# Kernel optimization log

Hardware: AMD Instinct MI355X
Metric: run time of the kernel (lower is better)

The kernel has to match this reference:

```python
import jax, jax.numpy as jnp
import numpy as np

N_SAMPLES = 16384
IN_FEATURES = 2048
N_COMPONENTS = 512
MAX_CROSS_TERMS = 512
# With n_components=512, max_cross_terms=512: interaction_depth=2 -> only pairwise
# cross terms, and n_pairwise = min(512*511//2, 512) = 512 (the first 512 pairs in
# lexicographic (i, j), i<j order -- exactly what the chunked torch loops produce).
_pi, _pj = np.triu_indices(N_COMPONENTS, k=1)  # lexicographic row-major order
PAIR_I = jnp.asarray(_pi[:MAX_CROSS_TERMS])
PAIR_J = jnp.asarray(_pj[:MAX_CROSS_TERMS])
SQRT_EPS = 1e-8


def setup_inputs() -> dict:
    key = jax.random.key(0)
    k1, k2 = jax.random.split(key)
    X = jax.random.normal(k1, (N_SAMPLES, IN_FEATURES), dtype=jnp.float32)
    projection = jax.random.normal(k2, (IN_FEATURES, N_COMPONENTS), dtype=jnp.float32) / np.sqrt(N_COMPONENTS)
    return {"X": X, "projection": projection}


def reference(X, projection):
    # Random projection: [N, in] @ [in, C] -> [N, C]
    Xp = X @ projection
    n = X.shape[0]
    bias = jnp.ones((n, 1), dtype=X.dtype)                 # 'bias' chunk
    p1 = Xp                                                # power_1
    p2 = Xp * Xp                                           # power_2
    p3 = p2 * Xp                                           # power_3
    pairs = Xp[:, PAIR_I] * Xp[:, PAIR_J]                  # pairwise cross terms
    sq = jnp.sqrt(jnp.abs(Xp) + SQRT_EPS)                  # sqrt features
    # Feature layout matches torch offsets: bias | p1 | p2 | p3 | cross | sqrt
    return jnp.concatenate([bias, p1, p2, p3, pairs, sq], axis=1)  # [N, 2561]
```

## Files before the change

kernel.cpp:

```cpp
#include <hip/hip_runtime.h>
#include <hip/hip_bf16.h>
#include <math.h>


typedef __attribute__((ext_vector_type(4))) float f32x4;
typedef __attribute__((ext_vector_type(8))) short bf16x8;

#define MM 16384
#define NN 512
#define KK 2048
#define OUTW 2561

#define BM 128
#define BN 128
#define BK 32
#define NT (KK / BK)

__device__ __forceinline__ short f2bf(float x) {
  union { __hip_bfloat16 b; short s; } u;
  u.b = __float2bfloat16(x);
  return u.s;
}

__device__ __forceinline__ bf16x8 cvt8(f32x4 a, f32x4 b) {
  bf16x8 r;
  r[0] = f2bf(a[0]); r[1] = f2bf(a[1]); r[2] = f2bf(a[2]); r[3] = f2bf(a[3]);
  r[4] = f2bf(b[0]); r[5] = f2bf(b[1]); r[6] = f2bf(b[2]); r[7] = f2bf(b[3]);
  return r;
}

__device__ __forceinline__ void gl_lds16(const void* g, void* l) {
  __builtin_amdgcn_global_load_lds((const __attribute__((address_space(1))) unsigned int*)g,
                                   (__attribute__((address_space(3))) unsigned int*)l, 16, 0, 0);
}

__global__ __launch_bounds__(256) void prep_b(const float* __restrict__ P, short* __restrict__ Bt) {
  __shared__ float ts[64][65];
  const int tid = threadIdx.x;
  const int k0 = (blockIdx.x >> 3) * 64;
  const int n0 = (blockIdx.x & 7) * 64;
#pragma unroll
  for (int j = 0; j < 16; ++j) {
    int idx = j * 256 + tid;
    int kr = idx >> 6, nc = idx & 63;
    ts[kr][nc] = P[(size_t)(k0 + kr) * NN + n0 + nc];
  }
  __syncthreads();
#pragma unroll
  for (int j = 0; j < 16; ++j) {
    int idx = j * 256 + tid;
    int nr = idx >> 6, kc = idx & 63;
    Bt[(size_t)(n0 + nr) * KK + k0 + kc] = f2bf(ts[kc][nr]);
  }
}

__global__ __launch_bounds__(256) void gemm4(const float* __restrict__ X,
                                             const short* __restrict__ Bt,
                                             float* __restrict__ out) {
  __shared__ short As[2][BM * BK];
  __shared__ short Bs[2][BN * BK];

  const int tid = threadIdx.x;
  const int wid = tid >> 6, lane = tid & 63;
  const int lrow = lane & 15, kh = lane >> 4;
  const int wr = wid >> 1, wc = wid & 1;

  const int bid = blockIdx.x;
  const int tile = (bid & 7) * 64 + (bid >> 3);
  const int m0 = (tile >> 2) * BM;
  const int n0 = (tile & 3) * BN;

  const int ar0 = tid >> 2, akq = tid & 3;
  const float* aG = X + (size_t)(m0 + ar0) * KK + akq * 8;
  int aoff[2];
#pragma unroll
  for (int j = 0; j < 2; ++j) {
    int row = j * 64 + ar0;
    aoff[j] = row * 32 + ((akq ^ ((row >> 1) & 3)) << 3);
  }

  const int kd = (lane & 3) ^ ((lane >> 3) & 3);
  const short* bG[2];
  int bOff[2];
#pragma unroll
  for (int p = 0; p < 2; ++p) {
    int R0 = (p * 4 + wid) * 16;
    bOff[p] = R0 * 32;
    bG[p] = Bt + (size_t)(n0 + R0 + (lane >> 2)) * KK + kd * 8;
  }

  f32x4 acc[4][4];
#pragma unroll
  for (int m = 0; m < 4; ++m)
#pragma unroll
    for (int n = 0; n < 4; ++n) acc[m][n] = (f32x4)0.0f;

#pragma unroll
  for (int p = 0; p < 2; ++p) gl_lds16(bG[p], &Bs[0][bOff[p]]);
  f32x4 a0 = *(const f32x4*)aG;
  f32x4 a1 = *(const f32x4*)(aG + 4);
  f32x4 a2 = *(const f32x4*)(aG + (size_t)64 * KK);
  f32x4 a3 = *(const f32x4*)(aG + (size_t)64 * KK + 4);
  *(bf16x8*)&As[0][aoff[0]] = cvt8(a0, a1);
  *(bf16x8*)&As[0][aoff[1]] = cvt8(a2, a3);
  a0 = *(const f32x4*)(aG + BK);
  a1 = *(const f32x4*)(aG + BK + 4);
  a2 = *(const f32x4*)(aG + (size_t)64 * KK + BK);
  a3 = *(const f32x4*)(aG + (size_t)64 * KK + BK + 4);
  __syncthreads();

  int cur = 0;
  for (int t = 0; t < NT; ++t) {
    if (t + 1 < NT) {
#pragma unroll
      for (int p = 0; p < 2; ++p) gl_lds16(bG[p] + (size_t)(t + 1) * BK, &Bs[cur ^ 1][bOff[p]]);
      *(bf16x8*)&As[cur ^ 1][aoff[0]] = cvt8(a0, a1);
      *(bf16x8*)&As[cur ^ 1][aoff[1]] = cvt8(a2, a3);
      int t2 = (t + 2 < NT) ? t + 2 : t;
      const float* ap = aG + (size_t)t2 * BK;
      a0 = *(const f32x4*)ap;
      a1 = *(const f32x4*)(ap + 4);
      a2 = *(const f32x4*)(ap + (size_t)64 * KK);
      a3 = *(const f32x4*)(ap + (size_t)64 * KK + 4);
    }
    const int sw = (lrow >> 1) & 3;
    bf16x8 af[4], bfr[4];
#pragma unroll
    for (int m = 0; m < 4; ++m) {
      int r = wr * 64 + m * 16 + lrow;
      af[m] = *(const bf16x8*)&As[cur][r * 32 + ((kh ^ sw) << 3)];
    }
#pragma unroll
    for (int n = 0; n < 4; ++n) {
      int r = wc * 64 + n * 16 + lrow;
      bfr[n] = *(const bf16x8*)&Bs[cur][r * 32 + ((kh ^ sw) << 3)];
    }
#pragma unroll
    for (int m = 0; m < 4; ++m)
#pragma unroll
      for (int n = 0; n < 4; ++n)
        acc[m][n] = __builtin_amdgcn_mfma_f32_16x16x32_bf16(af[m], bfr[n], acc[m][n], 0, 0, 0);
    __syncthreads();
    cur ^= 1;
  }

#pragma unroll
  for (int m = 0; m < 4; ++m)
#pragma unroll
    for (int n = 0; n < 4; ++n)
#pragma unroll
      for (int r = 0; r < 4; ++r) {
        int row = m0 + wr * 64 + m * 16 + kh * 4 + r;
        int col = n0 + wc * 64 + n * 16 + lrow;
        out[(size_t)row * OUTW + 1 + col] = acc[m][n][r];
      }
}

__global__ __launch_bounds__(512) void epi_k(float* __restrict__ out) {
  const int r = blockIdx.x;
  const int c = threadIdx.x;
  float* row = out + (size_t)r * OUTW;
  __shared__ float s[NN];
  float xp = row[1 + c];
  s[c] = xp;
  __syncthreads();
  float p2 = xp * xp;
  float p3 = p2 * xp;
  float sq = sqrtf(fabsf(xp) + 1e-8f);
  float pr = (c < 511) ? s[0] * s[c + 1] : s[1] * s[2];
  if (c == 0) row[0] = 1.0f;
  row[513 + c] = p2;
  row[1025 + c] = p3;
  row[1537 + c] = pr;
  row[2049 + c] = sq;
}

#define FBM 128
#define FBN 128
#define FPAD 40

__global__ __launch_bounds__(256) void gemm_k(const float* __restrict__ A,
                                              const float* __restrict__ B,
                                              float* __restrict__ out) {
  __shared__ __align__(16) short Asf[FBM][FPAD];
  __shared__ __align__(16) short Bsf[FBN][FPAD];
  const int tid = threadIdx.x;
  const int bx = blockIdx.x;
  const int m0 = (bx >> 2) * FBM;
  const int n0 = (bx & 3) * FBN;
  const int wid = tid >> 6, lane = tid & 63;
  const int wr = wid >> 1, wc = wid & 1;
  const int lrow = lane & 15, kh = lane >> 4;
  f32x4 acc[4][4];
#pragma unroll
  for (int i = 0; i < 4; i++)
#pragma unroll
    for (int j = 0; j < 4; j++) acc[i][j] = (f32x4)0.0f;
  for (int k0 = 0; k0 < KK; k0 += BK) {
#pragma unroll
    for (int i = 0; i < 4; i++) {
      int fid = i * 256 + tid;
      int ar = fid >> 3, ac = (fid & 7) << 2;
      f32x4 v = *(const f32x4*)(A + (size_t)(m0 + ar) * KK + (k0 + ac));
      short h0 = f2bf(v[0]), h1 = f2bf(v[1]), h2 = f2bf(v[2]), h3 = f2bf(v[3]);
      Asf[ar][ac] = h0; Asf[ar][ac + 1] = h1; Asf[ar][ac + 2] = h2; Asf[ar][ac + 3] = h3;
    }
#pragma unroll
    for (int i = 0; i < 4; i++) {
      int fid = i * 256 + tid;
      int br = fid >> 5, bc = (fid & 31) << 2;
      f32x4 v = *(const f32x4*)(B + (size_t)(k0 + br) * NN + (n0 + bc));
#pragma unroll
      for (int j = 0; j < 4; j++) Bsf[bc + j][br] = f2bf(v[j]);
    }
    __syncthreads();
    bf16x8 af[4], bf[4];
#pragma unroll
    for (int m = 0; m < 4; m++) af[m] = *(const bf16x8*)&Asf[wr * 64 + m * 16 + lrow][kh * 8];
#pragma unroll
    for (int n = 0; n < 4; n++) bf[n] = *(const bf16x8*)&Bsf[wc * 64 + n * 16 + lrow][kh * 8];
#pragma unroll
    for (int m = 0; m < 4; m++)
#pragma unroll
      for (int n = 0; n < 4; n++)
        acc[m][n] = __builtin_amdgcn_mfma_f32_16x16x32_bf16(af[m], bf[n], acc[m][n], 0, 0, 0);
    __syncthreads();
  }
#pragma unroll
  for (int m = 0; m < 4; m++)
#pragma unroll
    for (int n = 0; n < 4; n++)
#pragma unroll
      for (int r = 0; r < 4; r++) {
        int row = m0 + wr * 64 + m * 16 + kh * 4 + r;
        int col = n0 + wc * 64 + n * 16 + lrow;
        out[(size_t)row * OUTW + 1 + col] = acc[m][n][r];
      }
}

extern "C" void kernel_launch(void* const* d_in, const int* in_sizes, int n_in,
                              void* d_out, int out_size, void* d_ws, size_t ws_size,
                              hipStream_t stream) {
  const float* X = (const float*)d_in[0];
  const float* P = (const float*)d_in[1];
  float* out = (float*)d_out;
  (void)in_sizes; (void)n_in; (void)out_size;

  if (ws_size >= (size_t)NN * KK * sizeof(short)) {
    short* Bt = (short*)d_ws;
    prep_b<<<dim3(256), dim3(256), 0, stream>>>(P, Bt);
    gemm4<<<dim3((MM / BM) * (NN / BN)), dim3(256), 0, stream>>>(X, Bt, out);
  } else {
    gemm_k<<<dim3(512), dim3(256), 0, stream>>>(X, P, out);
  }
  epi_k<<<dim3(MM), dim3(512), 0, stream>>>(out);
}
```

Baseline: 127.6 us.

## Stream fp32 A tiles directly to LDS with triple-buffered async pipeline

The GEMM kernel now loads the fp32 X tiles straight into LDS with global_load_lds instead of through registers, and converts them to bf16 when reading fragments out of LDS. Both operand buffers become a three-stage ring with explicit vmcnt waits and one barrier per iteration, so two tiles are in flight while one is computed. The aim is to hide global-load latency and cut the register traffic and conversion work between loads and stores. In exchange LDS use grows (fp32 A, three stages), the conversion is repeated on each fragment read, and correctness depends on the hand-written waitcnt counts.

```diff
diff --git a/kernel.cpp b/kernel.cpp
--- a/kernel.cpp
+++ b/kernel.cpp
@@ -54,11 +54,11 @@
   }
 }
 
-__global__ __launch_bounds__(256) void gemm4(const float* __restrict__ X,
+__global__ __launch_bounds__(256) void gemm5(const float* __restrict__ X,
                                              const short* __restrict__ Bt,
                                              float* __restrict__ out) {
-  __shared__ short As[2][BM * BK];
-  __shared__ short Bs[2][BN * BK];
+  __shared__ float Asf[3][BM * BK];
+  __shared__ short Bsf[3][BN * BK];
 
   const int tid = threadIdx.x;
   const int wid = tid >> 6, lane = tid & 63;
@@ -70,23 +70,37 @@
   const int m0 = (tile >> 2) * BM;
   const int n0 = (tile & 3) * BN;
 
-  const int ar0 = tid >> 2, akq = tid & 3;
-  const float* aG = X + (size_t)(m0 + ar0) * KK + akq * 8;
-  int aoff[2];
-#pragma unroll
-  for (int j = 0; j < 2; ++j) {
-    int row = j * 64 + ar0;
-    aoff[j] = row * 32 + ((akq ^ ((row >> 1) & 3)) << 3);
-  }
-
+  const float* aSrc[4];
+  int aDst[4];
+#pragma unroll
+  for (int q = 0; q < 4; ++q) {
+    int inst = wid * 4 + q;
+    int row = inst * 8 + (lane >> 3);
+    int slot = (lane & 7) ^ ((lane >> 3) & 7);
+    aSrc[q] = X + (size_t)(m0 + row) * KK + slot * 4;
+    aDst[q] = inst * 256;
+  }
   const int kd = (lane & 3) ^ ((lane >> 3) & 3);
-  const short* bG[2];
-  int bOff[2];
+  const short* bSrc[2];
+  int bDst[2];
 #pragma unroll
   for (int p = 0; p < 2; ++p) {
     int R0 = (p * 4 + wid) * 16;
-    bOff[p] = R0 * 32;
-    bG[p] = Bt + (size_t)(n0 + R0 + (lane >> 2)) * KK + kd * 8;
+    bDst[p] = R0 * 32;
+    bSrc[p] = Bt + (size_t)(n0 + R0 + (lane >> 2)) * KK + kd * 8;
+  }
+
+  int offA[4][2], offB[4];
+#pragma unroll
+  for (int m = 0; m < 4; ++m) {
+    int r = wr * 64 + m * 16 + lrow;
+    offA[m][0] = r * 32 + (((2 * kh) ^ (r & 7)) << 2);
+    offA[m][1] = r * 32 + (((2 * kh + 1) ^ (r & 7)) << 2);
+  }
+#pragma unroll
+  for (int n = 0; n < 4; ++n) {
+    int r = wc * 64 + n * 16 + lrow;
+    offB[n] = r * 32 + ((kh ^ ((r >> 1) & 3)) << 3);
   }
 
   f32x4 acc[4][4];
@@ -95,54 +109,53 @@
 #pragma unroll
     for (int n = 0; n < 4; ++n) acc[m][n] = (f32x4)0.0f;
 
-#pragma unroll
-  for (int p = 0; p < 2; ++p) gl_lds16(bG[p], &Bs[0][bOff[p]]);
-  f32x4 a0 = *(const f32x4*)aG;
-  f32x4 a1 = *(const f32x4*)(aG + 4);
-  f32x4 a2 = *(const f32x4*)(aG + (size_t)64 * KK);
-  f32x4 a3 = *(const f32x4*)(aG + (size_t)64 * KK + 4);
-  *(bf16x8*)&As[0][aoff[0]] = cvt8(a0, a1);
-  *(bf16x8*)&As[0][aoff[1]] = cvt8(a2, a3);
-  a0 = *(const f32x4*)(aG + BK);
-  a1 = *(const f32x4*)(aG + BK + 4);
-  a2 = *(const f32x4*)(aG + (size_t)64 * KK + BK);
-  a3 = *(const f32x4*)(aG + (size_t)64 * KK + BK + 4);
-  __syncthreads();
-
-  int cur = 0;
-  for (int t = 0; t < NT; ++t) {
-    if (t + 1 < NT) {
-#pragma unroll
-      for (int p = 0; p < 2; ++p) gl_lds16(bG[p] + (size_t)(t + 1) * BK, &Bs[cur ^ 1][bOff[p]]);
-      *(bf16x8*)&As[cur ^ 1][aoff[0]] = cvt8(a0, a1);
-      *(bf16x8*)&As[cur ^ 1][aoff[1]] = cvt8(a2, a3);
-      int t2 = (t + 2 < NT) ? t + 2 : t;
-      const float* ap = aG + (size_t)t2 * BK;
-      a0 = *(const f32x4*)ap;
-      a1 = *(const f32x4*)(ap + 4);
-      a2 = *(const f32x4*)(ap + (size_t)64 * KK);
-      a3 = *(const f32x4*)(ap + (size_t)64 * KK + 4);
+  auto compute = [&](int b) {
+    const float* ab = &Asf[b][0];
+    const short* bb = &Bsf[b][0];
+    bf16x8 af[4], bfr[4];
+#pragma unroll
+    for (int m = 0; m < 4; ++m) {
+      f32x4 lo = *(const f32x4*)(ab + offA[m][0]);
+      f32x4 hi = *(const f32x4*)(ab + offA[m][1]);
+      af[m] = cvt8(lo, hi);
     }
-    const int sw = (lrow >> 1) & 3;
-    bf16x8 af[4], bfr[4];
-#pragma unroll
-    for (int m = 0; m < 4; ++m) {
-      int r = wr * 64 + m * 16 + lrow;
-      af[m] = *(const bf16x8*)&As[cur][r * 32 + ((kh ^ sw) << 3)];
-    }
-#pragma unroll
-    for (int n = 0; n < 4; ++n) {
-      int r = wc * 64 + n * 16 + lrow;
-      bfr[n] = *(const bf16x8*)&Bs[cur][r * 32 + ((kh ^ sw) << 3)];
-    }
+#pragma unroll
+    for (int n = 0; n < 4; ++n) bfr[n] = *(const bf16x8*)(bb + offB[n]);
 #pragma unroll
     for (int m = 0; m < 4; ++m)
 #pragma unroll
       for (int n = 0; n < 4; ++n)
         acc[m][n] = __builtin_amdgcn_mfma_f32_16x16x32_bf16(af[m], bfr[n], acc[m][n], 0, 0, 0);
-    __syncthreads();
-    cur ^= 1;
-  }
+  };
+
+#pragma unroll
+  for (int q = 0; q < 4; ++q) gl_lds16(aSrc[q], &Asf[0][aDst[q]]);
+#pragma unroll
+  for (int p = 0; p < 2; ++p) gl_lds16(bSrc[p], &Bsf[0][bDst[p]]);
+#pragma unroll
+  for (int q = 0; q < 4; ++q) gl_lds16(aSrc[q] + BK, &Asf[1][aDst[q]]);
+#pragma unroll
+  for (int p = 0; p < 2; ++p) gl_lds16(bSrc[p] + BK, &Bsf[1][bDst[p]]);
+
+  int b0 = 0;
+  for (int t = 0; t < NT - 2; ++t) {
+    asm volatile("s_waitcnt vmcnt(6)" ::: "memory");
+    __builtin_amdgcn_s_barrier();
+    int b2 = b0 + 2; if (b2 >= 3) b2 -= 3;
+#pragma unroll
+    for (int q = 0; q < 4; ++q) gl_lds16(aSrc[q] + (size_t)(t + 2) * BK, &Asf[b2][aDst[q]]);
+#pragma unroll
+    for (int p = 0; p < 2; ++p) gl_lds16(bSrc[p] + (size_t)(t + 2) * BK, &Bsf[b2][bDst[p]]);
+    compute(b0);
+    b0 = (b0 == 2) ? 0 : b0 + 1;
+  }
+  asm volatile("s_waitcnt vmcnt(6)" ::: "memory");
+  __builtin_amdgcn_s_barrier();
+  compute(b0);
+  b0 = (b0 == 2) ? 0 : b0 + 1;
+  asm volatile("s_waitcnt vmcnt(0)" ::: "memory");
+  __builtin_amdgcn_s_barrier();
+  compute(b0);
 
 #pragma unroll
   for (int m = 0; m < 4; ++m)
@@ -249,7 +262,7 @@
   if (ws_size >= (size_t)NN * KK * sizeof(short)) {
     short* Bt = (short*)d_ws;
     prep_b<<<dim3(256), dim3(256), 0, stream>>>(P, Bt);
-    gemm4<<<dim3((MM / BM) * (NN / BN)), dim3(256), 0, stream>>>(X, Bt, out);
+    gemm5<<<dim3((MM / BM) * (NN / BN)), dim3(256), 0, stream>>>(X, Bt, out);
   } else {
     gemm_k<<<dim3(512), dim3(256), 0, stream>>>(X, P, out);
   }
```

After: 154.3 us. +21.0%, slower.

## Split GEMM K dimension in two and reduce partials in epilogue

Applied to the files above, without the earlier changes.

The GEMM now runs 1024 blocks, each covering half of K, and writes its partial sums into the p1 and p2 regions of the output row. The epilogue adds the two partials before computing the features and writes the summed p1 back. This doubles the block count so more CUs are busy and each block's serial K loop is half as long. The cost is extra global traffic for the partial writes and re-reads, plus one more store per element in the epilogue.

```diff
diff --git a/kernel.cpp b/kernel.cpp
--- a/kernel.cpp
+++ b/kernel.cpp
@@ -14,7 +14,8 @@
 #define BM 128
 #define BN 128
 #define BK 32
-#define NT (KK / BK)
+#define KH (KK / 2)
+#define NT2 (KH / BK)
 
 __device__ __forceinline__ short f2bf(float x) {
   union { __hip_bfloat16 b; short s; } u;
@@ -54,7 +55,7 @@
   }
 }
 
-__global__ __launch_bounds__(256) void gemm4(const float* __restrict__ X,
+__global__ __launch_bounds__(256) void gemm8(const float* __restrict__ X,
                                              const short* __restrict__ Bt,
                                              float* __restrict__ out) {
   __shared__ short As[2][BM * BK];
@@ -66,12 +67,15 @@
   const int wr = wid >> 1, wc = wid & 1;
 
   const int bid = blockIdx.x;
-  const int tile = (bid & 7) * 64 + (bid >> 3);
+  const int s = (bid & 7) * 128 + (bid >> 3);
+  const int ks = s >> 9;
+  const int tile = s & 511;
   const int m0 = (tile >> 2) * BM;
   const int n0 = (tile & 3) * BN;
+  const int kb = ks * KH;
 
   const int ar0 = tid >> 2, akq = tid & 3;
-  const float* aG = X + (size_t)(m0 + ar0) * KK + akq * 8;
+  const float* aG = X + (size_t)(m0 + ar0) * KK + kb + akq * 8;
   int aoff[2];
 #pragma unroll
   for (int j = 0; j < 2; ++j) {
@@ -86,7 +90,7 @@
   for (int p = 0; p < 2; ++p) {
     int R0 = (p * 4 + wid) * 16;
     bOff[p] = R0 * 32;
-    bG[p] = Bt + (size_t)(n0 + R0 + (lane >> 2)) * KK + kd * 8;
+    bG[p] = Bt + (size_t)(n0 + R0 + (lane >> 2)) * KK + kb + kd * 8;
   }
 
   f32x4 acc[4][4];
@@ -110,13 +114,13 @@
   __syncthreads();
 
   int cur = 0;
-  for (int t = 0; t < NT; ++t) {
-    if (t + 1 < NT) {
+  for (int t = 0; t < NT2; ++t) {
+    if (t + 1 < NT2) {
 #pragma unroll
       for (int p = 0; p < 2; ++p) gl_lds16(bG[p] + (size_t)(t + 1) * BK, &Bs[cur ^ 1][bOff[p]]);
       *(bf16x8*)&As[cur ^ 1][aoff[0]] = cvt8(a0, a1);
       *(bf16x8*)&As[cur ^ 1][aoff[1]] = cvt8(a2, a3);
-      int t2 = (t + 2 < NT) ? t + 2 : t;
+      int t2 = (t + 2 < NT2) ? t + 2 : t;
       const float* ap = aG + (size_t)t2 * BK;
       a0 = *(const f32x4*)ap;
       a1 = *(const f32x4*)(ap + 4);
@@ -152,16 +156,16 @@
       for (int r = 0; r < 4; ++r) {
         int row = m0 + wr * 64 + m * 16 + kh * 4 + r;
         int col = n0 + wc * 64 + n * 16 + lrow;
-        out[(size_t)row * OUTW + 1 + col] = acc[m][n][r];
+        out[(size_t)row * OUTW + 1 + ks * NN + col] = acc[m][n][r];
       }
 }
 
-__global__ __launch_bounds__(512) void epi_k(float* __restrict__ out) {
+__global__ __launch_bounds__(512) void epi2_k(float* __restrict__ out) {
   const int r = blockIdx.x;
   const int c = threadIdx.x;
   float* row = out + (size_t)r * OUTW;
   __shared__ float s[NN];
-  float xp = row[1 + c];
+  float xp = row[1 + c] + row[513 + c];
   s[c] = xp;
   __syncthreads();
   float p2 = xp * xp;
@@ -169,6 +173,7 @@
   float sq = sqrtf(fabsf(xp) + 1e-8f);
   float pr = (c < 511) ? s[0] * s[c + 1] : s[1] * s[2];
   if (c == 0) row[0] = 1.0f;
+  row[1 + c] = xp;
   row[513 + c] = p2;
   row[1025 + c] = p3;
   row[1537 + c] = pr;
@@ -238,6 +243,25 @@
       }
 }
 
+__global__ __launch_bounds__(512) void epi_k(float* __restrict__ out) {
+  const int r = blockIdx.x;
+  const int c = threadIdx.x;
+  float* row = out + (size_t)r * OUTW;
+  __shared__ float s[NN];
+  float xp = row[1 + c];
+  s[c] = xp;
+  __syncthreads();
+  float p2 = xp * xp;
+  float p3 = p2 * xp;
+  float sq = sqrtf(fabsf(xp) + 1e-8f);
+  float pr = (c < 511) ? s[0] * s[c + 1] : s[1] * s[2];
+  if (c == 0) row[0] = 1.0f;
+  row[513 + c] = p2;
+  row[1025 + c] = p3;
+  row[1537 + c] = pr;
+  row[2049 + c] = sq;
+}
+
 extern "C" void kernel_launch(void* const* d_in, const int* in_sizes, int n_in,
                               void* d_out, int out_size, void* d_ws, size_t ws_size,
                               hipStream_t stream) {
@@ -249,9 +273,10 @@
   if (ws_size >= (size_t)NN * KK * sizeof(short)) {
     short* Bt = (short*)d_ws;
     prep_b<<<dim3(256), dim3(256), 0, stream>>>(P, Bt);
-    gemm4<<<dim3((MM / BM) * (NN / BN)), dim3(256), 0, stream>>>(X, Bt, out);
+    gemm8<<<dim3(1024), dim3(256), 0, stream>>>(X, Bt, out);
+    epi2_k<<<dim3(MM), dim3(512), 0, stream>>>(out);
   } else {
     gemm_k<<<dim3(512), dim3(256), 0, stream>>>(X, P, out);
-  }
-  epi_k<<<dim3(MM), dim3(512), 0, stream>>>(out);
-}
+    epi_k<<<dim3(MM), dim3(512), 0, stream>>>(out);
+  }
+}
```

After: 142.2 us. 1.11x slower.
